# Kernel optimization log

Hardware: AMD Instinct MI355X
Metric: run time of the kernel (lower is better)

## Reference

```python
import jax, jax.numpy as jnp
import numpy as np

# HEncLayer (demucs-style, freq mode): Conv2d kernel (8,1) stride (4,1) pad (2,0)
# -> GELU -> 1x1 'rewrite' conv to 2*out channels -> GLU over channels.

def _henc(x, w_conv, b_conv, w_rw, b_rw):
    y = jax.lax.conv_general_dilated(
        x, w_conv, window_strides=(4, 1), padding=[(2, 2), (0, 0)],
        dimension_numbers=("NCHW", "OIHW", "NCHW"))
    y = jax.nn.gelu(y + b_conv[None, :, None, None])
    z = jax.lax.conv_general_dilated(
        y, w_rw, window_strides=(1, 1), padding=[(0, 0), (0, 0)],
        dimension_numbers=("NCHW", "OIHW", "NCHW"))
    z = z + b_rw[None, :, None, None]
    a, b = jnp.split(z, 2, axis=1)  # GLU
    return a * jax.nn.sigmoid(b)


def setup_inputs() -> dict:
    key = jax.random.key(0)
    ks = jax.random.split(key, 6)
    init = lambda k, shape, fan: jax.random.normal(k, shape, jnp.float32) / np.sqrt(fan)
    x = jax.random.normal(ks[0], (8, 2, 2048, 256), jnp.float32)
    w1 = init(ks[1], (48, 2, 8, 1), 2 * 8); b1 = jnp.zeros((48,), jnp.float32)
    w2 = init(ks[2], (96, 48, 1, 1), 48);   b2 = jnp.zeros((96,), jnp.float32)
    w3 = init(ks[3], (96, 48, 8, 1), 48 * 8); b3 = jnp.zeros((96,), jnp.float32)
    w4 = init(ks[4], (192, 96, 1, 1), 96);  b4 = jnp.zeros((192,), jnp.float32)
    codebook = jax.random.normal(ks[5], (1024, 96), jnp.float32)  # codebook_size=1024, dim=96
    return {"x": x, "w1": w1, "b1": b1, "w2": w2, "b2": b2,
            "w3": w3, "b3": b3, "w4": w4, "b4": b4, "codebook": codebook}


def reference(x, w1, b1, w2, b2, w3, b3, w4, b4, codebook):
    # downsample: [8,2,2048,256] -> [8,48,512,256] -> [8,96,128,256]
    y = _henc(_henc(x, w1, b1, w2, b2), w3, b3, w4, b4)
    B, C, Fr, T = y.shape
    beforvq = y
    flat = y.reshape(B, C, Fr * T).transpose(0, 2, 1)  # [B, N, C]
    # squared euclidean distance to codebook: [B, N, K]
    d = (jnp.sum(flat * flat, axis=-1, keepdims=True)
         - 2.0 * jnp.einsum("bnd,kd->bnk", flat, codebook)
         + jnp.sum(codebook * codebook, axis=-1))
    indices = jnp.argmin(d, axis=-1)            # [B, N]
    q = codebook[indices]                        # gather: [B, N, C]
    # straight-through estimator (vector-quantize-pytorch semantics)
    latent = flat + jax.lax.stop_gradient(q - flat)
    latent = latent.transpose(0, 2, 1).reshape(B, C, Fr, T)
    return latent, indices, beforvq
```

## Files before the change

### kernel.cpp

```cpp
#include <hip/hip_runtime.h>
#include <math.h>


#define H1IN 2048
#define H1OUT 512
#define H2IN 512
#define H2OUT 128
#define TT 256
#define NPTS 32768
#define LAT_ELEMS 25165824
#define IDX_ELEMS 262144

typedef unsigned int uint;
typedef unsigned short ushort_t;
typedef __attribute__((ext_vector_type(8))) short bf16x8;
typedef __attribute__((ext_vector_type(4))) float f32x4;

__device__ __forceinline__ ushort_t f2bf(float x) {
    uint u = __float_as_uint(x);
    return (ushort_t)((u + 0x7fffu + ((u >> 16) & 1u)) >> 16);
}
__device__ __forceinline__ float bf2f(ushort_t h) {
    return __uint_as_float((uint)h << 16);
}

__global__ __launch_bounds__(256) void prep_kernel(
    const float* __restrict__ w1, const float* __restrict__ w2,
    const float* __restrict__ w3, const float* __restrict__ w4,
    const float* __restrict__ cb,
    float* __restrict__ w1t, float* __restrict__ w2t,
    float* __restrict__ w3t, float* __restrict__ w4t,
    float* __restrict__ cnorm)
{
    int i = blockIdx.x * 256 + threadIdx.x;
    if (i < 768) {
        int oc = i % 48; int r = i / 48;
        w1t[i] = w1[(oc * 2 + (r >> 3)) * 8 + (r & 7)];
    } else if (i < 5376) {
        int j = i - 768;
        int oc = j % 96, c = j / 96;
        w2t[j] = w2[oc * 48 + c];
    } else if (i < 42240) {
        int j = i - 5376;
        int oc = j % 96; int r = j / 96;
        w3t[j] = w3[(oc * 48 + (r >> 3)) * 8 + (r & 7)];
    } else if (i < 60672) {
        int j = i - 42240;
        int oc = j % 192, c = j / 192;
        w4t[j] = w4[oc * 96 + c];
    } else if (i < 61696) {
        int k = i - 60672;
        const float* cp = cb + (size_t)k * 96;
        double s = 0.0;
        for (int d = 0; d < 96; d++) s += (double)cp[d] * (double)cp[d];
        cnorm[k] = (float)s;
    }
}

__device__ __forceinline__ float gelu_tanh(float v) {
    float u = 0.7978845608028654f * (v + 0.044715f * v * v * v);
    return 0.5f * v * (1.f + tanhf(u));
}

__global__ __launch_bounds__(256, 2) void henc1_kernel(
    const float* __restrict__ x, const float* __restrict__ w1t,
    const float* __restrict__ b1, const float* __restrict__ w2t,
    const float* __restrict__ b2, float* __restrict__ y1)
{
    __shared__ float gs[48 * 256];
    int bh = blockIdx.x;
    int ho = bh & 511, b = bh >> 9;
    int t = threadIdx.x;

    float g[48];
#pragma unroll
    for (int oc = 0; oc < 48; oc++) g[oc] = b1[oc];

    const float* xb = x + (size_t)b * 2 * H1IN * TT;
    int hbase = ho * 4 - 2;
    for (int ci = 0; ci < 2; ci++) {
        for (int kh = 0; kh < 8; kh++) {
            int hi = hbase + kh;
            float v = (hi >= 0 && hi < H1IN) ? xb[((size_t)ci * H1IN + hi) * TT + t] : 0.f;
            const float* wp = w1t + (ci * 8 + kh) * 48;
#pragma unroll
            for (int oc = 0; oc < 48; oc++) g[oc] = fmaf(v, wp[oc], g[oc]);
        }
    }
#pragma unroll
    for (int oc = 0; oc < 48; oc++) gs[oc * 256 + t] = gelu_tanh(g[oc]);

    float z[96];
#pragma unroll
    for (int oc = 0; oc < 96; oc++) z[oc] = b2[oc];
    for (int c = 0; c < 48; c++) {
        float v = gs[c * 256 + t];
        const float* wp = w2t + c * 96;
#pragma unroll
        for (int oc = 0; oc < 96; oc++) z[oc] = fmaf(v, wp[oc], z[oc]);
    }

    float* yb = y1 + (size_t)b * 48 * H1OUT * TT + (size_t)ho * TT + t;
#pragma unroll
    for (int co = 0; co < 48; co++) {
        float o = z[co] / (1.f + expf(-z[co + 48]));
        yb[(size_t)co * H1OUT * TT] = o;
    }
}

__global__ __launch_bounds__(256, 2) void conv2a_kernel(
    const float* __restrict__ y1, const float* __restrict__ w3t,
    const float* __restrict__ b3, float* __restrict__ g2)
{
    int bh = blockIdx.x;
    int ho = bh & 127, b = bh >> 7;
    int t = threadIdx.x;

    float g[96];
#pragma unroll
    for (int oc = 0; oc < 96; oc++) g[oc] = b3[oc];

    const float* xb = y1 + (size_t)b * 48 * H2IN * TT;
    int hbase = ho * 4 - 2;
    for (int kh = 0; kh < 8; kh++) {
        int hi = hbase + kh;
        if (hi < 0 || hi >= H2IN) continue;
        const float* xr = xb + (size_t)hi * TT + t;
        for (int ci = 0; ci < 48; ci++) {
            float v = xr[(size_t)ci * H2IN * TT];
            const float* wp = w3t + (ci * 8 + kh) * 96;
#pragma unroll
            for (int oc = 0; oc < 96; oc++) g[oc] = fmaf(v, wp[oc], g[oc]);
        }
    }

    float* gp = g2 + (size_t)b * 96 * NPTS + (size_t)ho * TT + t;
#pragma unroll
    for (int oc = 0; oc < 96; oc++) gp[(size_t)oc * NPTS] = gelu_tanh(g[oc]);
}

__global__ __launch_bounds__(256, 2) void rw2b_kernel(
    const float* __restrict__ g2, const float* __restrict__ w4t,
    const float* __restrict__ b4, float* __restrict__ outv,
    const float* __restrict__ cb,
    ushort_t* __restrict__ fh, ushort_t* __restrict__ fl,
    ushort_t* __restrict__ cbh, ushort_t* __restrict__ cbl)
{
    int i = blockIdx.x * 256 + threadIdx.x;
    if (i < 98304) {
        float xv = cb[i];
        ushort_t h = f2bf(xv);
        cbh[i] = h;
        cbl[i] = f2bf(xv - bf2f(h));
    }

    int b = i >> 15, p = i & 32767;
    const float* gp = g2 + (size_t)b * 96 * NPTS + p;
    float* op = outv + (size_t)b * 96 * NPTS + p;

    for (int half = 0; half < 2; half++) {
        float za[48], zb[48];
#pragma unroll
        for (int j = 0; j < 48; j++) {
            za[j] = b4[half * 48 + j];
            zb[j] = b4[96 + half * 48 + j];
        }
        for (int c = 0; c < 96; c++) {
            float v = gp[(size_t)c * NPTS];
            const float* wp = w4t + c * 192;
#pragma unroll
            for (int j = 0; j < 48; j++) {
                za[j] = fmaf(v, wp[half * 48 + j], za[j]);
                zb[j] = fmaf(v, wp[96 + half * 48 + j], zb[j]);
            }
        }
        uint* fhp = (uint*)(fh + (size_t)i * 96 + half * 48);
        uint* flp = (uint*)(fl + (size_t)i * 96 + half * 48);
#pragma unroll
        for (int q = 0; q < 24; q++) {
            float o0 = za[2 * q]     / (1.f + expf(-zb[2 * q]));
            float o1 = za[2 * q + 1] / (1.f + expf(-zb[2 * q + 1]));
            op[(size_t)(half * 48 + 2 * q)     * NPTS] = o0;
            op[(size_t)(half * 48 + 2 * q + 1) * NPTS] = o1;
            ushort_t h0 = f2bf(o0); ushort_t l0 = f2bf(o0 - bf2f(h0));
            ushort_t h1 = f2bf(o1); ushort_t l1 = f2bf(o1 - bf2f(h1));
            fhp[q] = (uint)h0 | ((uint)h1 << 16);
            flp[q] = (uint)l0 | ((uint)l1 << 16);
        }
    }
}

__global__ __launch_bounds__(256, 3) void vqm_kernel(
    const float* __restrict__ bq,
    const ushort_t* __restrict__ fh, const ushort_t* __restrict__ fl,
    const ushort_t* __restrict__ cbh, const ushort_t* __restrict__ cbl,
    const float* __restrict__ cb, const float* __restrict__ cnorm,
    float* __restrict__ latent, float* __restrict__ idxf)
{
    __shared__ float mbuf[4][16][8];
    int tid = threadIdx.x;
    int lane = tid & 63;
    int wid = __builtin_amdgcn_readfirstlane(tid >> 6);
    int lrow = lane & 15, lgrp = lane >> 4;
    int gp0 = blockIdx.x * 64;
    int b = gp0 >> 15, p0 = gp0 & 32767;
    int pbase = gp0 + wid * 16;

    bf16x8 ah[3], al[3];
    {
        const ushort_t* ph = fh + (size_t)(pbase + lrow) * 96 + 8 * lgrp;
        const ushort_t* pl = fl + (size_t)(pbase + lrow) * 96 + 8 * lgrp;
#pragma unroll
        for (int kk = 0; kk < 3; kk++) {
            ah[kk] = *(const bf16x8*)(ph + kk * 32);
            al[kk] = *(const bf16x8*)(pl + kk * 32);
        }
    }

    float bs[4][4]; int bk[4][4];
#pragma unroll
    for (int r = 0; r < 4; r++)
#pragma unroll
        for (int j = 0; j < 4; j++) { bs[r][j] = 3.402823466e+38f; bk[r][j] = 0x7fffffff; }

    const ushort_t* qh = cbh + (size_t)lrow * 96 + 8 * lgrp;
    const ushort_t* ql = cbl + (size_t)lrow * 96 + 8 * lgrp;
    const float* cnp = cnorm + lrow;

    bf16x8 nbh0 = *(const bf16x8*)(qh);
    bf16x8 nbh1 = *(const bf16x8*)(qh + 32);
    bf16x8 nbh2 = *(const bf16x8*)(qh + 64);
    bf16x8 nbl0 = *(const bf16x8*)(ql);
    bf16x8 nbl1 = *(const bf16x8*)(ql + 32);
    bf16x8 nbl2 = *(const bf16x8*)(ql + 64);
    float ncn = *cnp;

#pragma unroll 1
    for (int ct = 0; ct < 64; ct++) {
        bf16x8 bh0 = nbh0, bh1 = nbh1, bh2 = nbh2;
        bf16x8 bl0 = nbl0, bl1 = nbl1, bl2 = nbl2;
        float cn = ncn;
        int code = ct * 16 + lrow;

        if (ct < 63) {
            qh += 16 * 96; ql += 16 * 96; cnp += 16;
            nbh0 = *(const bf16x8*)(qh);
            nbh1 = *(const bf16x8*)(qh + 32);
            nbh2 = *(const bf16x8*)(qh + 64);
            nbl0 = *(const bf16x8*)(ql);
            nbl1 = *(const bf16x8*)(ql + 32);
            nbl2 = *(const bf16x8*)(ql + 64);
            ncn = *cnp;
        }

        f32x4 acc = {0.f, 0.f, 0.f, 0.f};
        acc = __builtin_amdgcn_mfma_f32_16x16x32_bf16(ah[0], bh0, acc, 0, 0, 0);
        acc = __builtin_amdgcn_mfma_f32_16x16x32_bf16(ah[1], bh1, acc, 0, 0, 0);
        acc = __builtin_amdgcn_mfma_f32_16x16x32_bf16(ah[2], bh2, acc, 0, 0, 0);
        acc = __builtin_amdgcn_mfma_f32_16x16x32_bf16(ah[0], bl0, acc, 0, 0, 0);
        acc = __builtin_amdgcn_mfma_f32_16x16x32_bf16(ah[1], bl1, acc, 0, 0, 0);
        acc = __builtin_amdgcn_mfma_f32_16x16x32_bf16(ah[2], bl2, acc, 0, 0, 0);
        acc = __builtin_amdgcn_mfma_f32_16x16x32_bf16(al[0], bh0, acc, 0, 0, 0);
        acc = __builtin_amdgcn_mfma_f32_16x16x32_bf16(al[1], bh1, acc, 0, 0, 0);
        acc = __builtin_amdgcn_mfma_f32_16x16x32_bf16(al[2], bh2, acc, 0, 0, 0);

#pragma unroll
        for (int r = 0; r < 4; r++) {
            float s = fmaf(-2.f, acc[r], cn);
            if (s < bs[r][3]) {
                bs[r][3] = s; bk[r][3] = code;
                if (bs[r][3] < bs[r][2]) {
                    float ts = bs[r][2]; bs[r][2] = bs[r][3]; bs[r][3] = ts;
                    int   tk = bk[r][2]; bk[r][2] = bk[r][3]; bk[r][3] = tk;
                    if (bs[r][2] < bs[r][1]) {
                        ts = bs[r][1]; bs[r][1] = bs[r][2]; bs[r][2] = ts;
                        tk = bk[r][1]; bk[r][1] = bk[r][2]; bk[r][2] = tk;
                        if (bs[r][1] < bs[r][0]) {
                            ts = bs[r][0]; bs[r][0] = bs[r][1]; bs[r][1] = ts;
                            tk = bk[r][0]; bk[r][0] = bk[r][1]; bk[r][1] = tk;
                        }
                    }
                }
            }
        }
    }

#define CSW(si, ki, sj, kj) { bool c_ = (sj < si) || (sj == si && kj < ki); \
        float ls_ = c_ ? sj : si; float hs_ = c_ ? si : sj;                 \
        int   lk_ = c_ ? kj : ki; int   hk_ = c_ ? ki : kj;                 \
        si = ls_; ki = lk_; sj = hs_; kj = hk_; }
#pragma unroll
    for (int m = 1; m <= 8; m <<= 1) {
#pragma unroll
        for (int r = 0; r < 4; r++) {
            float os0 = __shfl_xor(bs[r][0], m), os1 = __shfl_xor(bs[r][1], m);
            float os2 = __shfl_xor(bs[r][2], m), os3 = __shfl_xor(bs[r][3], m);
            int   ok0 = __shfl_xor(bk[r][0], m), ok1 = __shfl_xor(bk[r][1], m);
            int   ok2 = __shfl_xor(bk[r][2], m), ok3 = __shfl_xor(bk[r][3], m);
            bool t0 = (bs[r][0] < os3) || (bs[r][0] == os3 && bk[r][0] < ok3);
            bool t1 = (bs[r][1] < os2) || (bs[r][1] == os2 && bk[r][1] < ok2);
            bool t2 = (bs[r][2] < os1) || (bs[r][2] == os1 && bk[r][2] < ok1);
            bool t3 = (bs[r][3] < os0) || (bs[r][3] == os0 && bk[r][3] < ok0);
            float L0s = t0 ? bs[r][0] : os3;  int L0k = t0 ? bk[r][0] : ok3;
            float L1s = t1 ? bs[r][1] : os2;  int L1k = t1 ? bk[r][1] : ok2;
            float L2s = t2 ? bs[r][2] : os1;  int L2k = t2 ? bk[r][2] : ok1;
            float L3s = t3 ? bs[r][3] : os0;  int L3k = t3 ? bk[r][3] : ok0;
            CSW(L0s, L0k, L2s, L2k); CSW(L1s, L1k, L3s, L3k);
            CSW(L0s, L0k, L1s, L1k); CSW(L2s, L2k, L3s, L3k);
            bs[r][0] = L0s; bk[r][0] = L0k; bs[r][1] = L1s; bk[r][1] = L1k;
            bs[r][2] = L2s; bk[r][2] = L2k; bs[r][3] = L3s; bk[r][3] = L3k;
        }
    }
#undef CSW

    if (lrow == 0) {
#pragma unroll
        for (int r = 0; r < 4; r++) {
            int pt = lgrp * 4 + r;
#pragma unroll
            for (int j = 0; j < 4; j++) {
                mbuf[wid][pt][j] = bs[r][j];
                mbuf[wid][pt][4 + j] = (float)bk[r][j];
            }
        }
    }
    __syncthreads();

    int p = lrow;
    int kj = (int)mbuf[wid][p][4 + lgrp];
    const float* fpt = bq + (size_t)b * 96 * NPTS + (p0 + wid * 16 + p);
    const float* cj = cb + (size_t)kj * 96;
    double sd = 0.0;
    for (int d = 0; d < 96; d++) {
        double fd = (double)fpt[(size_t)d * NPTS];
        double xv = (double)cj[d];
        sd = fma(xv, xv - 2.0 * fd, sd);
    }
#pragma unroll
    for (int m = 16; m <= 32; m <<= 1) {
        double so = __shfl_xor(sd, m);
        int    ko = __shfl_xor(kj, m);
        if (so < sd || (so == sd && ko < kj)) { sd = so; kj = ko; }
    }
    if (lgrp == 0) idxf[gp0 + wid * 16 + p] = (float)kj;

    const float* cbest = cb + (size_t)kj * 96;
    float* lp = latent + (size_t)b * 96 * NPTS + (p0 + wid * 16 + p);
#pragma unroll
    for (int i = 0; i < 24; i++) {
        int c = lgrp * 24 + i;
        lp[(size_t)c * NPTS] = cbest[c];
    }
}

extern "C" void kernel_launch(void* const* d_in, const int* in_sizes, int n_in,
                              void* d_out, int out_size, void* d_ws, size_t ws_size,
                              hipStream_t stream) {
    const float* x  = (const float*)d_in[0];
    const float* w1 = (const float*)d_in[1];
    const float* b1 = (const float*)d_in[2];
    const float* w2 = (const float*)d_in[3];
    const float* b2 = (const float*)d_in[4];
    const float* w3 = (const float*)d_in[5];
    const float* b3 = (const float*)d_in[6];
    const float* w4 = (const float*)d_in[7];
    const float* b4 = (const float*)d_in[8];
    const float* cb = (const float*)d_in[9];

    float* ws    = (float*)d_ws;
    float* y1    = ws;
    float* w1t   = ws + 50331648;
    float* w2t   = w1t + 768;
    float* w3t   = w2t + 4608;
    float* w4t   = w3t + 36864;
    float* cnorm = w4t + 18432;

    ushort_t* fh  = (ushort_t*)ws;
    ushort_t* fl  = (ushort_t*)(ws + 12582912);
    ushort_t* cbh = (ushort_t*)(ws + 25165824);
    ushort_t* cbl = (ushort_t*)(ws + 25165824 + 49152);

    float* out    = (float*)d_out;
    float* latent = out;
    float* idxf   = out + LAT_ELEMS;
    float* bq     = out + LAT_ELEMS + IDX_ELEMS;
    float* g2     = latent;

    prep_kernel<<<241, 256, 0, stream>>>(w1, w2, w3, w4, cb, w1t, w2t, w3t, w4t, cnorm);
    henc1_kernel<<<8 * 512, 256, 0, stream>>>(x, w1t, b1, w2t, b2, y1);
    conv2a_kernel<<<8 * 128, 256, 0, stream>>>(y1, w3t, b3, g2);
    rw2b_kernel<<<1024, 256, 0, stream>>>(g2, w4t, b4, bq, cb, fh, fl, cbh, cbl);
    vqm_kernel<<<4096, 256, 0, stream>>>(bq, fh, fl, cbh, cbl, cb, cnorm, latent, idxf);
}
```

Baseline: 1.423 ms.

## Restructure henc1 to recompute GELU per pass, dropping shared memory and registers

The first-layer kernel no longer stages the 48 GELU activations in shared memory or holds 96 accumulators per thread. It keeps the 16 input taps in registers and splits the output channels into three passes of 16 GLU pairs, recomputing the conv+GELU activations inside each pass. Launch bounds rise to 4 blocks per SM to exploit the lower register and LDS footprint. This trades three times the first-conv and GELU (tanh) arithmetic for higher occupancy and no LDS traffic.

Result: faster. 1.395 ms (-2.0%).

```diff
diff --git a/kernel.cpp b/kernel.cpp
--- a/kernel.cpp
+++ b/kernel.cpp
@@ -62,49 +62,57 @@
     return 0.5f * v * (1.f + tanhf(u));
 }
 
-__global__ __launch_bounds__(256, 2) void henc1_kernel(
+__global__ __launch_bounds__(256, 4) void henc1_kernel(
     const float* __restrict__ x, const float* __restrict__ w1t,
     const float* __restrict__ b1, const float* __restrict__ w2t,
     const float* __restrict__ b2, float* __restrict__ y1)
 {
-    __shared__ float gs[48 * 256];
     int bh = blockIdx.x;
     int ho = bh & 511, b = bh >> 9;
     int t = threadIdx.x;
 
-    float g[48];
-#pragma unroll
-    for (int oc = 0; oc < 48; oc++) g[oc] = b1[oc];
-
     const float* xb = x + (size_t)b * 2 * H1IN * TT;
     int hbase = ho * 4 - 2;
+    float xv[16];
+#pragma unroll
     for (int ci = 0; ci < 2; ci++) {
+#pragma unroll
         for (int kh = 0; kh < 8; kh++) {
             int hi = hbase + kh;
-            float v = (hi >= 0 && hi < H1IN) ? xb[((size_t)ci * H1IN + hi) * TT + t] : 0.f;
-            const float* wp = w1t + (ci * 8 + kh) * 48;
-#pragma unroll
-            for (int oc = 0; oc < 48; oc++) g[oc] = fmaf(v, wp[oc], g[oc]);
-        }
-    }
-#pragma unroll
-    for (int oc = 0; oc < 48; oc++) gs[oc * 256 + t] = gelu_tanh(g[oc]);
-
-    float z[96];
-#pragma unroll
-    for (int oc = 0; oc < 96; oc++) z[oc] = b2[oc];
-    for (int c = 0; c < 48; c++) {
-        float v = gs[c * 256 + t];
-        const float* wp = w2t + c * 96;
-#pragma unroll
-        for (int oc = 0; oc < 96; oc++) z[oc] = fmaf(v, wp[oc], z[oc]);
+            xv[ci * 8 + kh] = (hi >= 0 && hi < H1IN)
+                ? xb[((size_t)ci * H1IN + hi) * TT + t] : 0.f;
+        }
     }
 
     float* yb = y1 + (size_t)b * 48 * H1OUT * TT + (size_t)ho * TT + t;
-#pragma unroll
-    for (int co = 0; co < 48; co++) {
-        float o = z[co] / (1.f + expf(-z[co + 48]));
-        yb[(size_t)co * H1OUT * TT] = o;
+
+#pragma unroll 1
+    for (int pass = 0; pass < 3; pass++) {
+        int co0 = pass * 16;
+        float za[16], zb[16];
+#pragma unroll
+        for (int j = 0; j < 16; j++) {
+            za[j] = b2[co0 + j];
+            zb[j] = b2[48 + co0 + j];
+        }
+#pragma unroll 1
+        for (int c = 0; c < 48; c++) {
+            float gc = b1[c];
+#pragma unroll
+            for (int i = 0; i < 16; i++) gc = fmaf(xv[i], w1t[i * 48 + c], gc);
+            gc = gelu_tanh(gc);
+            const float* wp = w2t + c * 96;
+#pragma unroll
+            for (int j = 0; j < 16; j++) {
+                za[j] = fmaf(gc, wp[co0 + j], za[j]);
+                zb[j] = fmaf(gc, wp[48 + co0 + j], zb[j]);
+            }
+        }
+#pragma unroll
+        for (int j = 0; j < 16; j++) {
+            float o = za[j] / (1.f + expf(-zb[j]));
+            yb[(size_t)(co0 + j) * H1OUT * TT] = o;
+        }
     }
 }
 
```
